# Kernel tuning notes

Hardware: AMD Instinct MI355X
Metric: run time of the kernel (lower is better)

## Reference

```python
import jax, jax.numpy as jnp
import numpy as np

N = 50000        # nodes
E = 1250000      # edges
B = 512          # graphs
DIN, DH, DOUT = 64, 64, 16


def setup_inputs() -> dict:
    key = jax.random.key(0)
    ks = jax.random.split(key, 8)
    s = lambda d: np.float32(1.0 / np.sqrt(d))
    return {
        "x": jax.random.normal(ks[0], (N, DIN), jnp.float32),
        "edge_index": jax.random.randint(ks[1], (2, E), 0, N, dtype=jnp.int32),
        "batch": jnp.sort(jax.random.randint(ks[2], (N,), 0, B, dtype=jnp.int32)),
        "W1": jax.random.normal(ks[3], (DH, DIN), jnp.float32) * s(DIN),
        "b1": jnp.zeros((DH,), jnp.float32),
        "W2": jax.random.normal(ks[4], (DH, DH), jnp.float32) * s(DH),
        "b2": jnp.zeros((DH,), jnp.float32),
        "W3": jax.random.normal(ks[5], (DH, DH), jnp.float32) * s(DH),
        "b3": jnp.zeros((DH,), jnp.float32),
        "Wl": jax.random.normal(ks[6], (DOUT, DH), jnp.float32) * s(DH),
        "bl": jnp.zeros((DOUT,), jnp.float32),
    }


def _gcn_conv(x, src, dst, norm, W, b, n):
    # PyG GCNConv: h = x W^T; out[i] = sum_{(j->i)} norm_ji * h[j] + b
    h = x @ W.T                                   # [N, DH]
    msg = h[src] * norm[:, None]                  # [E+N, DH] gather
    return jax.ops.segment_sum(msg, dst, num_segments=n) + b


def reference(x, edge_index, batch, W1, b1, W2, b2, W3, b3, Wl, bl):
    n = x.shape[0]
    loop = jnp.arange(n, dtype=edge_index.dtype)
    # add self-loops (PyG GCNConv default add_self_loops=True)
    src = jnp.concatenate([edge_index[0], loop])
    dst = jnp.concatenate([edge_index[1], loop])
    # symmetric normalization: deg^{-1/2}[src] * deg^{-1/2}[dst]
    deg = jax.ops.segment_sum(jnp.ones_like(src, jnp.float32), dst, num_segments=n)
    dinv = jax.lax.rsqrt(deg)                     # deg >= 1 thanks to self-loops
    norm = dinv[src] * dinv[dst]

    h = x
    for W, b in ((W1, b1), (W2, b2), (W3, b3)):
        h = jax.nn.relu(_gcn_conv(h, src, dst, norm, W, b, n))

    # global mean pool over each graph
    sums = jax.ops.segment_sum(h, batch, num_segments=B)          # [B, DH]
    cnts = jax.ops.segment_sum(jnp.ones((n,), jnp.float32), batch, num_segments=B)
    pooled = sums / jnp.maximum(cnts, 1.0)[:, None]
    # dropout p=0.5 is identity in eval mode
    return pooled @ Wl.T + bl                                     # [B, DOUT]
```

## Files before the change

### kernel.cpp

```cpp
#include <hip/hip_runtime.h>
#include <hip/hip_fp16.h>


#define CAPB 3072
#define BINTILE 4096

__global__ __launch_bounds__(256) void init_kernel(int* __restrict__ fctr) {
    int idx = blockIdx.x * blockDim.x + threadIdx.x;
    if (idx < 512) fctr[idx] = 0;
}

__global__ __launch_bounds__(256) void bin512_kernel(const int* __restrict__ src,
                                                     const int* __restrict__ dst,
                                                     int* __restrict__ fctr,
                                                     int2* __restrict__ recs2,
                                                     int e, int n) {
    __shared__ int lcnt[512], gbase[512];
    int tid = threadIdx.x;
    int s0  = blockIdx.x * BINTILE;
    lcnt[tid] = 0;
    lcnt[tid + 256] = 0;
    __syncthreads();
    int dv[16], bk[16];
#pragma unroll
    for (int k = 0; k < 16; ++k) {
        int i = s0 + tid + k * 256;
        if (i < e) {
            dv[k] = dst[i];
            bk[k] = (int)((512LL * dv[k]) / n);
            atomicAdd(&lcnt[bk[k]], 1);
        } else {
            bk[k] = -1;
        }
    }
    __syncthreads();
#pragma unroll
    for (int j = 0; j < 2; ++j) {
        int b = tid + j * 256;
        gbase[b] = b * CAPB + atomicAdd(&fctr[b], lcnt[b]);
        lcnt[b]  = 0;
    }
    __syncthreads();
#pragma unroll
    for (int k = 0; k < 16; ++k) {
        if (bk[k] >= 0) {
            int i = s0 + tid + k * 256;
            int p = gbase[bk[k]] + atomicAdd(&lcnt[bk[k]], 1);
            if (p < (bk[k] + 1) * CAPB) recs2[p] = make_int2(src[i], dv[k]);
        }
    }
}

__global__ __launch_bounds__(64) void scan512_kernel(const int* __restrict__ fctr,
                                                     int* __restrict__ fbase) {
    int tid = threadIdx.x;
    int carry = 0;
    for (int b0 = 0; b0 < 512; b0 += 64) {
        int v    = fctr[b0 + tid];
        int orig = v;
        for (int d = 1; d < 64; d <<= 1) {
            int t = __shfl_up(v, d, 64);
            if (tid >= d) v += t;
        }
        fbase[b0 + tid] = carry + v - orig;
        carry += __shfl(v, 63, 64);
    }
}

__global__ __launch_bounds__(256) void sortfill_kernel(const int2* __restrict__ recs2,
                                                       const int* __restrict__ fctr,
                                                       const int* __restrict__ fbase,
                                                       int* __restrict__ rp,
                                                       float* __restrict__ dinv,
                                                       int* __restrict__ csr, int n) {
    __shared__ int hist[128];
    __shared__ int lofs[129];
    __shared__ int stage[4096];
    int g   = blockIdx.x;
    int N0  = (int)(((long long)n * g + 511) / 512);
    int N1  = (int)(((long long)n * (g + 1) + 511) / 512);
    int nn  = N1 - N0;
    int tid = threadIdx.x;
    if (tid < 128) hist[tid] = 0;
    __syncthreads();
    const int2* my = recs2 + (size_t)g * CAPB;
    int total = min(fctr[g], CAPB);
    for (int i = tid; i < total; i += 256)
        atomicAdd(&hist[my[i].y - N0], 1);
    __syncthreads();
    if (tid == 0) {
        int acc = 0;
        for (int k = 0; k < nn; ++k) { lofs[k] = acc; acc += hist[k]; }
        lofs[nn] = acc;
    }
    __syncthreads();
    if (tid < 128) hist[tid] = 0;
    __syncthreads();
    int base = fbase[g];
    for (int i = tid; i < total; i += 256) {
        int2 rec = my[i];
        int  li  = rec.y - N0;
        int  pos = lofs[li] + atomicAdd(&hist[li], 1);
        stage[pos] = rec.x;
    }
    __syncthreads();
    for (int j = tid; j < total; j += 256) csr[base + j] = stage[j];
    if (tid < nn) {
        rp[N0 + tid]   = base + lofs[tid];
        int deg        = lofs[tid + 1] - lofs[tid];
        dinv[N0 + tid] = rsqrtf((float)(deg + 1));
    }
    if (g == 511 && tid == 0) rp[n] = base + total;
}

__global__ __launch_bounds__(256) void mm_kernel(const float* __restrict__ h,
                                                 const float* __restrict__ W,
                                                 const float* __restrict__ dinv,
                                                 __half* __restrict__ t, int n) {
    __shared__ float hs[64 * 64];
    int tid  = threadIdx.x;
    int lane = tid & 63;
    int wave = tid >> 6;
    int base = blockIdx.x * 64;

    float4 wreg[16];
    const float4* W4 = (const float4*)(W + lane * 64);
#pragma unroll
    for (int q = 0; q < 16; ++q) wreg[q] = W4[q];

    int nrows = min(64, n - base);
    const float4* h4  = (const float4*)(h + (size_t)base * 64);
    float4*       hs4 = (float4*)hs;
    for (int idx = tid; idx < nrows * 16; idx += 256) hs4[idx] = h4[idx];
    __syncthreads();

    for (int r = wave * 16; r < wave * 16 + 16; ++r) {
        int i = base + r;
        if (i >= n) break;
        const float4* row = (const float4*)(hs + r * 64);
        float acc = 0.0f;
#pragma unroll
        for (int q = 0; q < 16; ++q) {
            float4 hv = row[q];
            acc += hv.x * wreg[q].x + hv.y * wreg[q].y +
                   hv.z * wreg[q].z + hv.w * wreg[q].w;
        }
        t[(size_t)i * 64 + lane] = __float2half(acc * dinv[i]);
    }
}

__global__ __launch_bounds__(256) void agg_kernel(const __half* __restrict__ t,
                                                  const int* __restrict__ rp,
                                                  const int* __restrict__ cs,
                                                  const float* __restrict__ dinv,
                                                  const float* __restrict__ bias,
                                                  float* __restrict__ hout, int n) {
    int gw   = (blockIdx.x * blockDim.x + threadIdx.x) >> 6;
    int lane = threadIdx.x & 63;
    if (gw >= n) return;
    int i   = gw;
    int grp = lane >> 4;
    int fo  = (lane & 15) << 2;
    int beg = rp[i];
    int end = rp[i + 1];

    float4 a0 = make_float4(0.f, 0.f, 0.f, 0.f);
    float4 a1 = a0, a2 = a0, a3 = a0;
    int e = beg + grp;
    for (; e + 12 < end; e += 16) {
        int s0 = cs[e];
        int s1 = cs[e + 4];
        int s2 = cs[e + 8];
        int s3 = cs[e + 12];
        uint2 u0 = *(const uint2*)(t + (size_t)s0 * 64 + fo);
        uint2 u1 = *(const uint2*)(t + (size_t)s1 * 64 + fo);
        uint2 u2 = *(const uint2*)(t + (size_t)s2 * 64 + fo);
        uint2 u3 = *(const uint2*)(t + (size_t)s3 * 64 + fo);
        float2 f;
        f = __half22float2(*(const __half2*)&u0.x); a0.x += f.x; a0.y += f.y;
        f = __half22float2(*(const __half2*)&u0.y); a0.z += f.x; a0.w += f.y;
        f = __half22float2(*(const __half2*)&u1.x); a1.x += f.x; a1.y += f.y;
        f = __half22float2(*(const __half2*)&u1.y); a1.z += f.x; a1.w += f.y;
        f = __half22float2(*(const __half2*)&u2.x); a2.x += f.x; a2.y += f.y;
        f = __half22float2(*(const __half2*)&u2.y); a2.z += f.x; a2.w += f.y;
        f = __half22float2(*(const __half2*)&u3.x); a3.x += f.x; a3.y += f.y;
        f = __half22float2(*(const __half2*)&u3.y); a3.z += f.x; a3.w += f.y;
    }
    for (; e < end; e += 4) {
        int s = cs[e];
        uint2 u = *(const uint2*)(t + (size_t)s * 64 + fo);
        float2 f;
        f = __half22float2(*(const __half2*)&u.x); a1.x += f.x; a1.y += f.y;
        f = __half22float2(*(const __half2*)&u.y); a1.z += f.x; a1.w += f.y;
    }
    float4 acc;
    acc.x = (a0.x + a1.x) + (a2.x + a3.x);
    acc.y = (a0.y + a1.y) + (a2.y + a3.y);
    acc.z = (a0.z + a1.z) + (a2.z + a3.z);
    acc.w = (a0.w + a1.w) + (a2.w + a3.w);
    acc.x += __shfl_xor(acc.x, 16, 64);
    acc.y += __shfl_xor(acc.y, 16, 64);
    acc.z += __shfl_xor(acc.z, 16, 64);
    acc.w += __shfl_xor(acc.w, 16, 64);
    acc.x += __shfl_xor(acc.x, 32, 64);
    acc.y += __shfl_xor(acc.y, 32, 64);
    acc.z += __shfl_xor(acc.z, 32, 64);
    acc.w += __shfl_xor(acc.w, 32, 64);
    if (grp == 0) {
        uint2 su = *(const uint2*)(t + (size_t)i * 64 + fo);
        float2 s01 = __half22float2(*(const __half2*)&su.x);
        float2 s23 = __half22float2(*(const __half2*)&su.y);
        float4 bv = *(const float4*)(bias + fo);
        float  dv = dinv[i];
        float4 o;
        o.x = fmaxf(fmaf(dv, acc.x + s01.x, bv.x), 0.0f);
        o.y = fmaxf(fmaf(dv, acc.y + s01.y, bv.y), 0.0f);
        o.z = fmaxf(fmaf(dv, acc.z + s23.x, bv.z), 0.0f);
        o.w = fmaxf(fmaf(dv, acc.w + s23.y, bv.w), 0.0f);
        *(float4*)(hout + (size_t)i * 64 + fo) = o;
    }
}

__global__ __launch_bounds__(256) void poolfinal_kernel(const float* __restrict__ h,
                                                        const int* __restrict__ batch,
                                                        const float* __restrict__ Wl,
                                                        const float* __restrict__ bl,
                                                        float* __restrict__ out,
                                                        int n) {
    __shared__ float red[4][64];
    int b    = blockIdx.x;
    int tid  = threadIdx.x;
    int lane = tid & 63;
    int w    = tid >> 6;
    int l = 0, r = n;
    while (l < r) { int m = (l + r) >> 1; if (batch[m] < b) l = m + 1; else r = m; }
    int lo = l;
    r = n;
    while (l < r) { int m = (l + r) >> 1; if (batch[m] < b + 1) l = m + 1; else r = m; }
    int hi = l;

    float acc = 0.0f;
    for (int i = lo + w; i < hi; i += 4) acc += h[(size_t)i * 64 + lane];
    red[w][lane] = acc;
    __syncthreads();
    if (w == 0) {
        float s = (red[0][lane] + red[1][lane]) + (red[2][lane] + red[3][lane]);
        float c = (float)(hi - lo);
        red[0][lane] = s / fmaxf(c, 1.0f);
    }
    __syncthreads();
    if (tid < 16) {
        float a = bl[tid];
        const float* wr = Wl + tid * 64;
#pragma unroll
        for (int k = 0; k < 64; ++k) a += red[0][k] * wr[k];
        out[b * 16 + tid] = a;
    }
}

extern "C" void kernel_launch(void* const* d_in, const int* in_sizes, int n_in,
                              void* d_out, int out_size, void* d_ws, size_t ws_size,
                              hipStream_t stream) {
    const float* x    = (const float*)d_in[0];
    const int*   ei   = (const int*)d_in[1];
    const int*   batch= (const int*)d_in[2];
    const float* W1   = (const float*)d_in[3];
    const float* b1   = (const float*)d_in[4];
    const float* W2   = (const float*)d_in[5];
    const float* b2   = (const float*)d_in[6];
    const float* W3   = (const float*)d_in[7];
    const float* b3   = (const float*)d_in[8];
    const float* Wl   = (const float*)d_in[9];
    const float* bl   = (const float*)d_in[10];
    float* out = (float*)d_out;

    const int n  = in_sizes[0] / 64;
    const int e  = in_sizes[1] / 2;
    const int nb = out_size / 16;

    const int* esrc = ei;
    const int* edst = ei + e;

    char* p = (char*)d_ws;
    auto carve = [&](size_t bytes) {
        char* r = p;
        p += (bytes + 255) & ~(size_t)255;
        return r;
    };
    size_t featBytes = (size_t)n * 64 * 4;
    size_t recsBytes = (size_t)512 * CAPB * 8;
    size_t bufBBytes = recsBytes > featBytes ? recsBytes : featBytes;

    float*  dinv = (float*)carve((size_t)n * 4);
    int*    rp   = (int*)  carve((size_t)(n + 1) * 4);
    int*    csr  = (int*)  carve((size_t)e * 4);
    __half* bufT = (__half*)carve((size_t)n * 64 * 2);
    float*  bufB = (float*)carve(bufBBytes);
    int*    fctr = (int*)  carve(512 * 4);
    int*    fbase= (int*)  carve(512 * 4);
    int2*   recs2 = (int2*)bufB;

    dim3 blk(256);
    int gBIN = (e + BINTILE - 1) / BINTILE;

    init_kernel<<<2, blk, 0, stream>>>(fctr);
    bin512_kernel<<<gBIN, blk, 0, stream>>>(esrc, edst, fctr, recs2, e, n);
    scan512_kernel<<<1, 64, 0, stream>>>(fctr, fbase);
    sortfill_kernel<<<512, blk, 0, stream>>>(recs2, fctr, fbase, rp, dinv, csr, n);

    int gMM  = (n + 63) / 64;
    int gAGG = (n + 3) / 4;

    mm_kernel<<<gMM, blk, 0, stream>>>(x, W1, dinv, bufT, n);
    agg_kernel<<<gAGG, blk, 0, stream>>>(bufT, rp, csr, dinv, b1, bufB, n);
    mm_kernel<<<gMM, blk, 0, stream>>>(bufB, W2, dinv, bufT, n);
    agg_kernel<<<gAGG, blk, 0, stream>>>(bufT, rp, csr, dinv, b2, bufB, n);
    mm_kernel<<<gMM, blk, 0, stream>>>(bufB, W3, dinv, bufT, n);
    agg_kernel<<<gAGG, blk, 0, stream>>>(bufT, rp, csr, dinv, b3, bufB, n);

    poolfinal_kernel<<<nb, blk, 0, stream>>>(bufB, batch, Wl, bl, out, n);
}
```

Measured before the change: 319.0 us.

## Fuse aggregation with next-layer matmul and fold bucket scan into sortfill

Layers 1 and 2 now aggregate neighbors and immediately apply the next layer's weight matrix within one kernel. Each aggregated row is staged through shared memory, and the result is written as dinv-scaled fp16 into a ping-pong buffer. This removes two mm kernel launches and the fp32 round trip of intermediate features through global memory. The separate scan kernel is also removed: each sortfill block recomputes its prefix base by a block reduction over the bucket counts. In exchange, every lane in the fused kernel reloads a 64-float row of W per node, and sortfill does redundant prefix work.

```diff
diff --git a/kernel.cpp b/kernel.cpp
--- a/kernel.cpp
+++ b/kernel.cpp
@@ -51,38 +51,32 @@
     }
 }
 
-__global__ __launch_bounds__(64) void scan512_kernel(const int* __restrict__ fctr,
-                                                     int* __restrict__ fbase) {
-    int tid = threadIdx.x;
-    int carry = 0;
-    for (int b0 = 0; b0 < 512; b0 += 64) {
-        int v    = fctr[b0 + tid];
-        int orig = v;
-        for (int d = 1; d < 64; d <<= 1) {
-            int t = __shfl_up(v, d, 64);
-            if (tid >= d) v += t;
-        }
-        fbase[b0 + tid] = carry + v - orig;
-        carry += __shfl(v, 63, 64);
-    }
-}
-
 __global__ __launch_bounds__(256) void sortfill_kernel(const int2* __restrict__ recs2,
                                                        const int* __restrict__ fctr,
-                                                       const int* __restrict__ fbase,
                                                        int* __restrict__ rp,
                                                        float* __restrict__ dinv,
                                                        int* __restrict__ csr, int n) {
     __shared__ int hist[128];
     __shared__ int lofs[129];
     __shared__ int stage[4096];
+    __shared__ int redbuf[256];
     int g   = blockIdx.x;
     int N0  = (int)(((long long)n * g + 511) / 512);
     int N1  = (int)(((long long)n * (g + 1) + 511) / 512);
     int nn  = N1 - N0;
     int tid = threadIdx.x;
+
+    int partial = 0;
+    for (int j = tid; j < g; j += 256) partial += min(fctr[j], CAPB);
+    redbuf[tid] = partial;
     if (tid < 128) hist[tid] = 0;
     __syncthreads();
+    for (int s = 128; s > 0; s >>= 1) {
+        if (tid < s) redbuf[tid] += redbuf[tid + s];
+        __syncthreads();
+    }
+    int base = redbuf[0];
+
     const int2* my = recs2 + (size_t)g * CAPB;
     int total = min(fctr[g], CAPB);
     for (int i = tid; i < total; i += 256)
@@ -96,7 +90,6 @@
     __syncthreads();
     if (tid < 128) hist[tid] = 0;
     __syncthreads();
-    int base = fbase[g];
     for (int i = tid; i < total; i += 256) {
         int2 rec = my[i];
         int  li  = rec.y - N0;
@@ -146,6 +139,97 @@
                    hv.z * wreg[q].z + hv.w * wreg[q].w;
         }
         t[(size_t)i * 64 + lane] = __float2half(acc * dinv[i]);
+    }
+}
+
+__global__ __launch_bounds__(256) void aggmm_kernel(const __half* __restrict__ t,
+                                                    const int* __restrict__ rp,
+                                                    const int* __restrict__ cs,
+                                                    const float* __restrict__ dinv,
+                                                    const float* __restrict__ bias,
+                                                    const float* __restrict__ Wn,
+                                                    __half* __restrict__ tout, int n) {
+    __shared__ float hrow[4][64];
+    int gw   = (blockIdx.x * blockDim.x + threadIdx.x) >> 6;
+    int lane = threadIdx.x & 63;
+    int wave = threadIdx.x >> 6;
+    bool active = (gw < n);
+    int i   = active ? gw : 0;
+    int grp = lane >> 4;
+    int fo  = (lane & 15) << 2;
+
+    if (active) {
+        int beg = rp[i];
+        int end = rp[i + 1];
+        float4 a0 = make_float4(0.f, 0.f, 0.f, 0.f);
+        float4 a1 = a0, a2 = a0, a3 = a0;
+        int e = beg + grp;
+        for (; e + 12 < end; e += 16) {
+            int s0 = cs[e];
+            int s1 = cs[e + 4];
+            int s2 = cs[e + 8];
+            int s3 = cs[e + 12];
+            uint2 u0 = *(const uint2*)(t + (size_t)s0 * 64 + fo);
+            uint2 u1 = *(const uint2*)(t + (size_t)s1 * 64 + fo);
+            uint2 u2 = *(const uint2*)(t + (size_t)s2 * 64 + fo);
+            uint2 u3 = *(const uint2*)(t + (size_t)s3 * 64 + fo);
+            float2 f;
+            f = __half22float2(*(const __half2*)&u0.x); a0.x += f.x; a0.y += f.y;
+            f = __half22float2(*(const __half2*)&u0.y); a0.z += f.x; a0.w += f.y;
+            f = __half22float2(*(const __half2*)&u1.x); a1.x += f.x; a1.y += f.y;
+            f = __half22float2(*(const __half2*)&u1.y); a1.z += f.x; a1.w += f.y;
+            f = __half22float2(*(const __half2*)&u2.x); a2.x += f.x; a2.y += f.y;
+            f = __half22float2(*(const __half2*)&u2.y); a2.z += f.x; a2.w += f.y;
+            f = __half22float2(*(const __half2*)&u3.x); a3.x += f.x; a3.y += f.y;
+            f = __half22float2(*(const __half2*)&u3.y); a3.z += f.x; a3.w += f.y;
+        }
+        for (; e < end; e += 4) {
+            int s = cs[e];
+            uint2 u = *(const uint2*)(t + (size_t)s * 64 + fo);
+            float2 f;
+            f = __half22float2(*(const __half2*)&u.x); a1.x += f.x; a1.y += f.y;
+            f = __half22float2(*(const __half2*)&u.y); a1.z += f.x; a1.w += f.y;
+        }
+        float4 acc;
+        acc.x = (a0.x + a1.x) + (a2.x + a3.x);
+        acc.y = (a0.y + a1.y) + (a2.y + a3.y);
+        acc.z = (a0.z + a1.z) + (a2.z + a3.z);
+        acc.w = (a0.w + a1.w) + (a2.w + a3.w);
+        acc.x += __shfl_xor(acc.x, 16, 64);
+        acc.y += __shfl_xor(acc.y, 16, 64);
+        acc.z += __shfl_xor(acc.z, 16, 64);
+        acc.w += __shfl_xor(acc.w, 16, 64);
+        acc.x += __shfl_xor(acc.x, 32, 64);
+        acc.y += __shfl_xor(acc.y, 32, 64);
+        acc.z += __shfl_xor(acc.z, 32, 64);
+        acc.w += __shfl_xor(acc.w, 32, 64);
+        if (grp == 0) {
+            uint2 su = *(const uint2*)(t + (size_t)i * 64 + fo);
+            float2 s01 = __half22float2(*(const __half2*)&su.x);
+            float2 s23 = __half22float2(*(const __half2*)&su.y);
+            float4 bv = *(const float4*)(bias + fo);
+            float  dv = dinv[i];
+            hrow[wave][fo + 0] = fmaxf(fmaf(dv, acc.x + s01.x, bv.x), 0.0f);
+            hrow[wave][fo + 1] = fmaxf(fmaf(dv, acc.y + s01.y, bv.y), 0.0f);
+            hrow[wave][fo + 2] = fmaxf(fmaf(dv, acc.z + s23.x, bv.z), 0.0f);
+            hrow[wave][fo + 3] = fmaxf(fmaf(dv, acc.w + s23.y, bv.w), 0.0f);
+        }
+    }
+    __syncthreads();
+    if (active) {
+        float4 wreg[16];
+        const float4* W4 = (const float4*)(Wn + lane * 64);
+#pragma unroll
+        for (int q = 0; q < 16; ++q) wreg[q] = W4[q];
+        const float4* hr = (const float4*)hrow[wave];
+        float acc2 = 0.0f;
+#pragma unroll
+        for (int q = 0; q < 16; ++q) {
+            float4 hv = hr[q];
+            acc2 += hv.x * wreg[q].x + hv.y * wreg[q].y +
+                    hv.z * wreg[q].z + hv.w * wreg[q].w;
+        }
+        tout[(size_t)i * 64 + lane] = __float2half(acc2 * dinv[i]);
     }
 }
 
@@ -291,31 +375,27 @@
     size_t recsBytes = (size_t)512 * CAPB * 8;
     size_t bufBBytes = recsBytes > featBytes ? recsBytes : featBytes;
 
-    float*  dinv = (float*)carve((size_t)n * 4);
-    int*    rp   = (int*)  carve((size_t)(n + 1) * 4);
-    int*    csr  = (int*)  carve((size_t)e * 4);
-    __half* bufT = (__half*)carve((size_t)n * 64 * 2);
-    float*  bufB = (float*)carve(bufBBytes);
-    int*    fctr = (int*)  carve(512 * 4);
-    int*    fbase= (int*)  carve(512 * 4);
+    float*  dinv  = (float*)carve((size_t)n * 4);
+    int*    rp    = (int*)  carve((size_t)(n + 1) * 4);
+    int*    csr   = (int*)  carve((size_t)e * 4);
+    __half* bufT  = (__half*)carve((size_t)n * 64 * 2);
+    __half* bufT2 = (__half*)carve((size_t)n * 64 * 2);
+    float*  bufB  = (float*)carve(bufBBytes);
+    int*    fctr  = (int*)  carve(512 * 4);
     int2*   recs2 = (int2*)bufB;
 
     dim3 blk(256);
     int gBIN = (e + BINTILE - 1) / BINTILE;
+    int gMM  = (n + 63) / 64;
+    int gAGG = (n + 3) / 4;
 
     init_kernel<<<2, blk, 0, stream>>>(fctr);
     bin512_kernel<<<gBIN, blk, 0, stream>>>(esrc, edst, fctr, recs2, e, n);
-    scan512_kernel<<<1, 64, 0, stream>>>(fctr, fbase);
-    sortfill_kernel<<<512, blk, 0, stream>>>(recs2, fctr, fbase, rp, dinv, csr, n);
-
-    int gMM  = (n + 63) / 64;
-    int gAGG = (n + 3) / 4;
+    sortfill_kernel<<<512, blk, 0, stream>>>(recs2, fctr, rp, dinv, csr, n);
 
     mm_kernel<<<gMM, blk, 0, stream>>>(x, W1, dinv, bufT, n);
-    agg_kernel<<<gAGG, blk, 0, stream>>>(bufT, rp, csr, dinv, b1, bufB, n);
-    mm_kernel<<<gMM, blk, 0, stream>>>(bufB, W2, dinv, bufT, n);
-    agg_kernel<<<gAGG, blk, 0, stream>>>(bufT, rp, csr, dinv, b2, bufB, n);
-    mm_kernel<<<gMM, blk, 0, stream>>>(bufB, W3, dinv, bufT, n);
+    aggmm_kernel<<<gAGG, blk, 0, stream>>>(bufT, rp, csr, dinv, b1, W2, bufT2, n);
+    aggmm_kernel<<<gAGG, blk, 0, stream>>>(bufT2, rp, csr, dinv, b2, W3, bufT, n);
     agg_kernel<<<gAGG, blk, 0, stream>>>(bufT, rp, csr, dinv, b3, bufB, n);
 
     poolfinal_kernel<<<nb, blk, 0, stream>>>(bufB, batch, Wl, bl, out, n);
```

After: 417.9 us. 31.0% more time.
